# Kernel tuning notes

Measured on AMD Instinct MI355X. Metric: run time of the kernel, lower is better.

## Reference

```python
import jax, jax.numpy as jnp
import numpy as np

H = 31   # hidden_size
IN = 36  # input_size
NC = 7   # num_classes
B = 1024
T = 512


def setup_inputs() -> dict:
    key = jax.random.key(0)
    ks = jax.random.split(key, 19)
    s = 1.0 / np.sqrt(H)  # PyTorch GRU init range
    u = lambda k, shape: jax.random.uniform(k, shape, jnp.float32, -s, s)
    inp = {"x": jax.random.normal(ks[0], (B, T, IN), jnp.float32)}
    i = 1
    for l, din in ((0, IN), (1, 2 * H)):
        for d in ("f", "b"):
            inp[f"W_ih_l{l}{d}"] = u(ks[i], (3 * H, din)); i += 1
            inp[f"W_hh_l{l}{d}"] = u(ks[i], (3 * H, H)); i += 1
            inp[f"b_ih_l{l}{d}"] = u(ks[i], (3 * H,)); i += 1
            inp[f"b_hh_l{l}{d}"] = u(ks[i], (3 * H,)); i += 1
    inp["fc_w"] = u(ks[17], (NC, 2 * H))
    inp["fc_b"] = u(ks[18], (NC,))
    return inp


def _gru_dir(x, Wih, Whh, bih, bhh, reverse):
    # x: [B,T,F]; precompute input-side gates for all timesteps in one GEMM
    xg = jnp.einsum('btf,gf->btg', x, Wih) + bih  # [B,T,3H]
    if reverse:
        xg = xg[:, ::-1]

    def step(h, xt):
        hg = h @ Whh.T + bhh                      # [B,3H]
        xr, xz, xn = jnp.split(xt, 3, axis=-1)    # PyTorch gate order: r,z,n
        hr, hz, hn = jnp.split(hg, 3, axis=-1)
        r = jax.nn.sigmoid(xr + hr)
        z = jax.nn.sigmoid(xz + hz)
        n = jnp.tanh(xn + r * hn)
        h_new = (1.0 - z) * n + z * h
        return h_new, h_new

    h0 = jnp.zeros((x.shape[0], Whh.shape[1]), x.dtype)
    _, ys = jax.lax.scan(step, h0, jnp.swapaxes(xg, 0, 1))  # [T,B,H]
    ys = jnp.swapaxes(ys, 0, 1)                              # [B,T,H]
    return ys[:, ::-1] if reverse else ys


def _forward(x, params, fc_w, fc_b):
    h = x
    for pf, pb in params:  # 2 layers (structural loop)
        yf = _gru_dir(h, *pf, reverse=False)
        yb = _gru_dir(h, *pb, reverse=True)
        h = jnp.concatenate([yf, yb], axis=-1)  # [B,T,2H]
    last = h[:, -1, :]                          # out[:, -1, :]
    return last @ fc_w.T + fc_b                 # [B,NC]


def reference(x, W_ih_l0f, W_hh_l0f, b_ih_l0f, b_hh_l0f,
              W_ih_l0b, W_hh_l0b, b_ih_l0b, b_hh_l0b,
              W_ih_l1f, W_hh_l1f, b_ih_l1f, b_hh_l1f,
              W_ih_l1b, W_hh_l1b, b_ih_l1b, b_hh_l1b,
              fc_w, fc_b):
    params = [((W_ih_l0f, W_hh_l0f, b_ih_l0f, b_hh_l0f),
               (W_ih_l0b, W_hh_l0b, b_ih_l0b, b_hh_l0b)),
              ((W_ih_l1f, W_hh_l1f, b_ih_l1f, b_hh_l1f),
               (W_ih_l1b, W_hh_l1b, b_ih_l1b, b_hh_l1b))]
    return _forward(x, params, fc_w, fc_b)
```

## Files before the change

### kernel.cpp

```cpp
#include <hip/hip_runtime.h>
#include <hip/hip_bf16.h>


#define NB 1024
#define NT 512
#define NH 31
#define NG 93
#define NC 7

__device__ __forceinline__ float sig_(float x) { return 1.f / (1.f + __expf(-x)); }
__device__ __forceinline__ float th_(float x)  { float e = __expf(2.f * x); return (e - 1.f) / (e + 1.f); }

__device__ __forceinline__ float tf_(float v) { return v; }
__device__ __forceinline__ float tf_(__hip_bfloat16 v) { return __bfloat162float(v); }

__device__ __forceinline__ void ldpair(const float* p, float& a, float& b) {
    float2 v = *(const float2*)p; a = v.x; b = v.y;
}
__device__ __forceinline__ void ldpair(const __hip_bfloat16* p, float& a, float& b) {
    ushort2 u = *(const ushort2*)p;
    a = __uint_as_float((unsigned)u.x << 16);
    b = __uint_as_float((unsigned)u.y << 16);
}
__device__ __forceinline__ void stoy(float* p, float v) { *p = v; }
__device__ __forceinline__ void stoy(__hip_bfloat16* p, float v) { *p = __float2bfloat16(v); }

#define PIN(v_) asm volatile("" : "+v"(v_))

#define LOADX(arr, ptr)                                                   \
    _Pragma("unroll") for (int k_ = 0; k_ < KH; k_ += 2)                  \
        ldpair((ptr) + k_, arr[k_], arr[k_ + 1])

#define GRU_STEP(XV)                                                      \
    do {                                                                  \
        const float4 g0 = *(const float4*)&hbuf[w][hlo + 0];              \
        const float4 g1 = *(const float4*)&hbuf[w][hlo + 4];              \
        const float4 g2 = *(const float4*)&hbuf[w][hlo + 8];              \
        const float4 g3 = *(const float4*)&hbuf[w][hlo + 12];             \
        float hv[16];                                                     \
        hv[0]=g0.x;  hv[1]=g0.y;  hv[2]=g0.z;  hv[3]=g0.w;                \
        hv[4]=g1.x;  hv[5]=g1.y;  hv[6]=g1.z;  hv[7]=g1.w;                \
        hv[8]=g2.x;  hv[9]=g2.y;  hv[10]=g2.z; hv[11]=g2.w;               \
        hv[12]=g3.x; hv[13]=g3.y; hv[14]=g3.z; hv[15]=g3.w;               \
        float ar = b_r, az = b_z, an = b_xn, ah = b_hn;                   \
        _Pragma("unroll") for (int k_ = 0; k_ < KH; ++k_) {               \
            ar = fmaf(Wxr[k_], XV[k_], ar);                               \
            az = fmaf(Wxz[k_], XV[k_], az);                               \
            an = fmaf(Wxn[k_], XV[k_], an);                               \
        }                                                                 \
        _Pragma("unroll") for (int k_ = 0; k_ < 16; ++k_) {               \
            ar = fmaf(Whr[k_], hv[k_], ar);                               \
            az = fmaf(Whz[k_], hv[k_], az);                               \
            ah = fmaf(Whn[k_], hv[k_], ah);                               \
        }                                                                 \
        ar += __shfl_xor(ar, 32, 64);                                     \
        az += __shfl_xor(az, 32, 64);                                     \
        an += __shfl_xor(an, 32, 64);                                     \
        ah += __shfl_xor(ah, 32, 64);                                     \
        const float r_ = sig_(ar);                                        \
        const float z_ = sig_(az);                                        \
        const float n_ = th_(an + r_ * ah);                               \
        h_prev = n_ + z_ * (h_prev - n_);                                 \
        if (half == 0 && j < NH) {                                        \
            hbuf[w][j] = h_prev;                                          \
            if (WRITE_Y) stoy(yp, h_prev);                                \
        }                                                                 \
    } while (0)

template<typename XT, typename YT, int DIN, int KH, bool WRITE_Y, bool WRITE_HF>
__device__ __forceinline__ void gru_scan_body(
    const XT* __restrict__ xin,
    const float* __restrict__ Wih, const float* __restrict__ Whh,
    const float* __restrict__ bih, const float* __restrict__ bhh,
    int dir, YT* __restrict__ y, float* __restrict__ hf)
{
    static_assert((KH & 1) == 0, "even KH");
    const int tid  = threadIdx.x;
    const int w    = tid >> 6;
    const int lane = tid & 63;
    const int half = lane >> 5;
    const int j    = lane & 31;
    const int jj   = j < NH ? j : NH - 1;
    const int b    = blockIdx.x * 4 + w;

    __shared__ __align__(16) float hbuf[4][32];
    if (lane < 32) hbuf[w][lane] = 0.f;
    __syncthreads();

    const int klo = half ? (DIN - KH) : 0;

    float Wxr[KH], Wxz[KH], Wxn[KH];
#pragma unroll
    for (int k = 0; k < KH; ++k) {
        const bool v = half ? true : (k < DIN - KH);
        Wxr[k] = v ? Wih[(0 * NH + jj) * DIN + klo + k] : 0.f;
        Wxz[k] = v ? Wih[(1 * NH + jj) * DIN + klo + k] : 0.f;
        Wxn[k] = v ? Wih[(2 * NH + jj) * DIN + klo + k] : 0.f;
        PIN(Wxr[k]); PIN(Wxz[k]); PIN(Wxn[k]);
    }
    const int hlo = half * 16;
    float Whr[16], Whz[16], Whn[16];
#pragma unroll
    for (int k = 0; k < 16; ++k) {
        const bool v = (hlo + k) < NH;
        Whr[k] = v ? Whh[(0 * NH + jj) * NH + hlo + k] : 0.f;
        Whz[k] = v ? Whh[(1 * NH + jj) * NH + hlo + k] : 0.f;
        Whn[k] = v ? Whh[(2 * NH + jj) * NH + hlo + k] : 0.f;
        PIN(Whr[k]); PIN(Whz[k]); PIN(Whn[k]);
    }
    float b_r = 0.f, b_z = 0.f, b_xn = 0.f, b_hn = 0.f;
    if (half == 0) {
        b_r  = bih[jj] + bhh[jj];
        b_z  = bih[NH + jj] + bhh[NH + jj];
        b_xn = bih[2 * NH + jj];
        b_hn = bhh[2 * NH + jj];
    }
    PIN(b_r); PIN(b_z); PIN(b_xn); PIN(b_hn);

    const XT* xrow = xin + (size_t)b * NT * DIN + klo
                   + (dir ? (size_t)(NT - 1) * DIN : 0);
    const ptrdiff_t xstep = dir ? -DIN : DIN;
    YT* yp = nullptr;
    ptrdiff_t ystep = 0;
    if (WRITE_Y) {
        yp = y + (size_t)b * NT * 62 + dir * NH + j
           + (dir ? (size_t)(NT - 1) * 62 : 0);
        ystep = dir ? -62 : 62;
    }

    float h_prev = 0.f;
    float xa[KH], xb[KH];
    LOADX(xa, xrow);
    const XT* xpre = xrow + xstep;

    for (int s = 0; s < NT; s += 2) {
        LOADX(xb, xpre);
        if (s + 2 < NT) xpre += xstep;
        GRU_STEP(xa);
        if (WRITE_Y) yp += ystep;
        LOADX(xa, xpre);
        if (s + 3 < NT) xpre += xstep;
        GRU_STEP(xb);
        if (WRITE_Y) yp += ystep;
    }
    if (WRITE_HF && half == 0 && j < NH) hf[b * NH + j] = h_prev;
}

template<typename YT>
__global__ void __launch_bounds__(256)
__attribute__((amdgpu_waves_per_eu(2, 2)))
gru_scan_l0(
    const float* __restrict__ x,
    const float* __restrict__ Wf, const float* __restrict__ Uf,
    const float* __restrict__ bf, const float* __restrict__ cf,
    const float* __restrict__ Wb, const float* __restrict__ Ub,
    const float* __restrict__ bb, const float* __restrict__ cb,
    YT* __restrict__ y)
{
    const int d = blockIdx.y;
    gru_scan_body<float, YT, 36, 18, true, false>(
        x, d ? Wb : Wf, d ? Ub : Uf, d ? bb : bf, d ? cb : cf, d, y, nullptr);
}

template<typename YT>
__global__ void __launch_bounds__(256)
__attribute__((amdgpu_waves_per_eu(1, 1)))
gru_scan_l1(
    const YT* __restrict__ y0,
    const float* __restrict__ W, const float* __restrict__ U,
    const float* __restrict__ bi, const float* __restrict__ bh,
    float* __restrict__ hf)
{
    gru_scan_body<YT, YT, 62, 32, false, true>(y0, W, U, bi, bh, 0, (YT*)nullptr, hf);
}

template<typename YT>
__global__ void __launch_bounds__(64, 4) gru_final(
    const YT* __restrict__ y0, const float* __restrict__ hf,
    const float* __restrict__ Wih1b, const float* __restrict__ bih1b,
    const float* __restrict__ bhh1b,
    const float* __restrict__ fcw, const float* __restrict__ fcb,
    float* __restrict__ out)
{
    const int b = blockIdx.x;
    const int lane = threadIdx.x;
    __shared__ float row[62];
    __shared__ float xg[NG];
    __shared__ float last[62];
    const YT* yl = y0 + ((size_t)b * NT + (NT - 1)) * 62;
    if (lane < 62) row[lane] = tf_(yl[lane]);
    __syncthreads();
    for (int g = lane; g < NG; g += 64) {
        float a = bih1b[g];
        const float* wr = Wih1b + g * 62;
#pragma unroll
        for (int k = 0; k < 62; ++k) a = fmaf(wr[k], row[k], a);
        xg[g] = a;
    }
    if (lane < NH) last[lane] = hf[b * NH + lane];
    __syncthreads();
    if (lane < NH) {
        const float r = sig_(xg[lane] + bhh1b[lane]);
        const float z = sig_(xg[NH + lane] + bhh1b[NH + lane]);
        const float n = th_(xg[2 * NH + lane] + r * bhh1b[2 * NH + lane]);
        last[NH + lane] = (1.f - z) * n;
    }
    __syncthreads();
    if (lane < NC) {
        float a = fcb[lane];
        const float* wr = fcw + lane * 62;
#pragma unroll
        for (int k = 0; k < 62; ++k) a = fmaf(wr[k], last[k], a);
        out[b * NC + lane] = a;
    }
}

extern "C" void kernel_launch(void* const* d_in, const int* in_sizes, int n_in,
                              void* d_out, int out_size, void* d_ws, size_t ws_size,
                              hipStream_t stream)
{
    const float* x     = (const float*)d_in[0];
    const float* Wih0f = (const float*)d_in[1];
    const float* Whh0f = (const float*)d_in[2];
    const float* bih0f = (const float*)d_in[3];
    const float* bhh0f = (const float*)d_in[4];
    const float* Wih0b = (const float*)d_in[5];
    const float* Whh0b = (const float*)d_in[6];
    const float* bih0b = (const float*)d_in[7];
    const float* bhh0b = (const float*)d_in[8];
    const float* Wih1f = (const float*)d_in[9];
    const float* Whh1f = (const float*)d_in[10];
    const float* bih1f = (const float*)d_in[11];
    const float* bhh1f = (const float*)d_in[12];
    const float* Wih1b = (const float*)d_in[13];
    const float* Whh1b = (const float*)d_in[14];
    const float* bih1b = (const float*)d_in[15];
    const float* bhh1b = (const float*)d_in[16];
    const float* fcw   = (const float*)d_in[17];
    const float* fcb   = (const float*)d_in[18];
    float* out = (float*)d_out;
    (void)Whh1b; (void)in_sizes; (void)n_in; (void)out_size;

    const size_t y0_elems  = (size_t)NB * NT * 62;
    const size_t hf_bytes  = (size_t)NB * NH * 4;
    const size_t need_f32  = y0_elems * 4 + 256 + hf_bytes;
    const size_t need_bf16 = y0_elems * 2 + 256 + hf_bytes;

    const dim3 blk(256);
    if (ws_size >= need_f32) {
        float* y0 = (float*)d_ws;
        float* hf = (float*)((char*)d_ws + ((y0_elems * 4 + 255) & ~(size_t)255));
        gru_scan_l0<float><<<dim3(NB / 4, 2), blk, 0, stream>>>(
            x, Wih0f, Whh0f, bih0f, bhh0f, Wih0b, Whh0b, bih0b, bhh0b, y0);
        gru_scan_l1<float><<<dim3(NB / 4, 1), blk, 0, stream>>>(
            y0, Wih1f, Whh1f, bih1f, bhh1f, hf);
        gru_final<float><<<dim3(NB), dim3(64), 0, stream>>>(
            y0, hf, Wih1b, bih1b, bhh1b, fcw, fcb, out);
    } else if (ws_size >= need_bf16) {
        __hip_bfloat16* y0 = (__hip_bfloat16*)d_ws;
        float* hf = (float*)((char*)d_ws + ((y0_elems * 2 + 255) & ~(size_t)255));
        gru_scan_l0<__hip_bfloat16><<<dim3(NB / 4, 2), blk, 0, stream>>>(
            x, Wih0f, Whh0f, bih0f, bhh0f, Wih0b, Whh0b, bih0b, bhh0b, y0);
        gru_scan_l1<__hip_bfloat16><<<dim3(NB / 4, 1), blk, 0, stream>>>(
            y0, Wih1f, Whh1f, bih1f, bhh1f, hf);
        gru_final<__hip_bfloat16><<<dim3(NB), dim3(64), 0, stream>>>(
            y0, hf, Wih1b, bih1b, bhh1b, fcw, fcb, out);
    }
}
```

Measured before the change: 571.1 us.

## Precompute input-gate projections in separate kernels and run a lean recurrent scan

```diff
diff --git a/kernel.cpp b/kernel.cpp
--- a/kernel.cpp
+++ b/kernel.cpp
@@ -7,6 +7,8 @@
 #define NH 31
 #define NG 93
 #define NC 7
+#define BT (NB * NT)
+#define XGP 96
 
 __device__ __forceinline__ float sig_(float x) { return 1.f / (1.f + __expf(-x)); }
 __device__ __forceinline__ float th_(float x)  { float e = __expf(2.f * x); return (e - 1.f) / (e + 1.f); }
@@ -24,6 +26,232 @@
 }
 __device__ __forceinline__ void stoy(float* p, float v) { *p = v; }
 __device__ __forceinline__ void stoy(__hip_bfloat16* p, float v) { *p = __float2bfloat16(v); }
+
+
+template<int DIN, int NDIR>
+__global__ void __launch_bounds__(256)
+__attribute__((amdgpu_waves_per_eu(1, 4)))
+gru_xg(const float* __restrict__ xin,
+       const float* __restrict__ W0, const float* __restrict__ bi0,
+       const float* __restrict__ W1, const float* __restrict__ bi1,
+       float* __restrict__ xg)
+{
+    __shared__ float tile[256 * DIN];
+    const int tid = threadIdx.x;
+    const size_t blk0 = (size_t)blockIdx.x * 256;
+
+    {
+        const float2* gsrc = (const float2*)(xin + blk0 * DIN);
+        float2* lds2 = (float2*)tile;
+#pragma unroll
+        for (int i = 0; i < DIN / 2; ++i)
+            lds2[tid + i * 256] = gsrc[tid + i * 256];
+    }
+    __syncthreads();
+
+    float xr[DIN];
+#pragma unroll
+    for (int k = 0; k < DIN; k += 2) {
+        float2 v = *(const float2*)&tile[tid * DIN + k];
+        xr[k] = v.x; xr[k + 1] = v.y;
+    }
+    const size_t row = blk0 + tid;
+
+#pragma unroll
+    for (int d = 0; d < NDIR; ++d) {
+        const float* __restrict__ W  = d ? W1 : W0;
+        const float* __restrict__ bi = d ? bi1 : bi0;
+        float* outp = xg + (d * (size_t)BT + row) * XGP;
+        for (int g = 0; g < NG - 1; g += 4) {
+            float a0 = bi[g], a1 = bi[g + 1], a2 = bi[g + 2], a3 = bi[g + 3];
+#pragma unroll
+            for (int k = 0; k < DIN; ++k) {
+                const float xv = xr[k];
+                a0 = fmaf(W[(g + 0) * DIN + k], xv, a0);
+                a1 = fmaf(W[(g + 1) * DIN + k], xv, a1);
+                a2 = fmaf(W[(g + 2) * DIN + k], xv, a2);
+                a3 = fmaf(W[(g + 3) * DIN + k], xv, a3);
+            }
+            float4 o; o.x = a0; o.y = a1; o.z = a2; o.w = a3;
+            *(float4*)(outp + g) = o;
+        }
+        {
+            float a = bi[NG - 1];
+#pragma unroll
+            for (int k = 0; k < DIN; ++k)
+                a = fmaf(W[(NG - 1) * DIN + k], xr[k], a);
+            outp[NG - 1] = a;
+        }
+    }
+}
+
+#define LDG3(R_, Z_, N_, P_)                                              \
+    do { R_ = (P_)[jj]; Z_ = (P_)[NH + jj]; N_ = (P_)[2 * NH + jj]; } while (0)
+
+#define ADVX()                                                            \
+    do { if (++tl < NT) xq += xqs; } while (0)
+
+#define LSTEP(XR_, XZ_, XN_)                                              \
+    do {                                                                  \
+        const float4 q0 = *(const float4*)&hbuf[w][hlo + 0];              \
+        const float4 q1 = *(const float4*)&hbuf[w][hlo + 4];              \
+        const float4 q2 = *(const float4*)&hbuf[w][hlo + 8];              \
+        const float4 q3 = *(const float4*)&hbuf[w][hlo + 12];             \
+        float hv[16];                                                     \
+        hv[0]=q0.x;  hv[1]=q0.y;  hv[2]=q0.z;  hv[3]=q0.w;                \
+        hv[4]=q1.x;  hv[5]=q1.y;  hv[6]=q1.z;  hv[7]=q1.w;                \
+        hv[8]=q2.x;  hv[9]=q2.y;  hv[10]=q2.z; hv[11]=q2.w;               \
+        hv[12]=q3.x; hv[13]=q3.y; hv[14]=q3.z; hv[15]=q3.w;               \
+        float ar = fmaf(hm, XR_, b_r);                                    \
+        float az = fmaf(hm, XZ_, b_z);                                    \
+        float an = hm * (XN_);                                            \
+        float ah = b_hn;                                                  \
+        _Pragma("unroll") for (int k_ = 0; k_ < 16; ++k_) {               \
+            ar = fmaf(Whr[k_], hv[k_], ar);                               \
+            az = fmaf(Whz[k_], hv[k_], az);                               \
+            ah = fmaf(Whn[k_], hv[k_], ah);                               \
+        }                                                                 \
+        ar += __shfl_xor(ar, 32, 64);                                     \
+        az += __shfl_xor(az, 32, 64);                                     \
+        an += __shfl_xor(an, 32, 64);                                     \
+        ah += __shfl_xor(ah, 32, 64);                                     \
+        const float r_ = sig_(ar);                                        \
+        const float z_ = sig_(az);                                        \
+        const float n_ = th_(an + r_ * ah);                               \
+        h_prev = n_ + z_ * (h_prev - n_);                                 \
+        if (half == 0 && j < NH) {                                        \
+            hbuf[w][j] = h_prev;                                          \
+            if (WRITE_Y) *yp = h_prev;                                    \
+        }                                                                 \
+        if (WRITE_Y) yp += ystep;                                         \
+    } while (0)
+
+template<bool WRITE_Y, bool WRITE_HF>
+__device__ __forceinline__ void gru_scan_lean_body(
+    const float* __restrict__ xgd,
+    const float* __restrict__ Whh, const float* __restrict__ bhh,
+    int dir, float* __restrict__ y, float* __restrict__ hf)
+{
+    const int tid  = threadIdx.x;
+    const int w    = tid >> 6;
+    const int lane = tid & 63;
+    const int half = lane >> 5;
+    const int j    = lane & 31;
+    const int jj   = j < NH ? j : NH - 1;
+    const int b    = blockIdx.x * 4 + w;
+
+    __shared__ __align__(16) float hbuf[4][32];
+    if (lane < 32) hbuf[w][lane] = 0.f;
+    __syncthreads();
+
+    const int hlo = half * 16;
+    float Whr[16], Whz[16], Whn[16];
+#pragma unroll
+    for (int k = 0; k < 16; ++k) {
+        const bool v = (hlo + k) < NH;
+        Whr[k] = v ? Whh[(0 * NH + jj) * NH + hlo + k] : 0.f;
+        Whz[k] = v ? Whh[(1 * NH + jj) * NH + hlo + k] : 0.f;
+        Whn[k] = v ? Whh[(2 * NH + jj) * NH + hlo + k] : 0.f;
+    }
+    float b_r = 0.f, b_z = 0.f, b_hn = 0.f;
+    if (half == 0) {
+        b_r  = bhh[jj];
+        b_z  = bhh[NH + jj];
+        b_hn = bhh[2 * NH + jj];
+    }
+    const float hm = (half == 0) ? 1.f : 0.f;
+
+    const float* xq = xgd + ((size_t)b * NT + (dir ? NT - 1 : 0)) * XGP;
+    const ptrdiff_t xqs = dir ? -XGP : XGP;
+    float* yp = nullptr;
+    ptrdiff_t ystep = 0;
+    if (WRITE_Y) {
+        yp = y + (size_t)b * NT * 62 + dir * NH + j
+           + (dir ? (size_t)(NT - 1) * 62 : 0);
+        ystep = dir ? -62 : 62;
+    }
+
+    float h_prev = 0.f;
+    int tl = 0;
+    float ra, za, na, rb, zb, nb, rc, zc, nc, rd, zd, nd;
+    LDG3(ra, za, na, xq); ADVX();
+    LDG3(rb, zb, nb, xq); ADVX();
+    LDG3(rc, zc, nc, xq); ADVX();
+
+    for (int it = 0; it < NT / 4; ++it) {
+        LDG3(rd, zd, nd, xq); ADVX();
+        LSTEP(ra, za, na);
+        LDG3(ra, za, na, xq); ADVX();
+        LSTEP(rb, zb, nb);
+        LDG3(rb, zb, nb, xq); ADVX();
+        LSTEP(rc, zc, nc);
+        LDG3(rc, zc, nc, xq); ADVX();
+        LSTEP(rd, zd, nd);
+    }
+    if (WRITE_HF && half == 0 && j < NH) hf[b * NH + j] = h_prev;
+}
+
+__global__ void __launch_bounds__(256)
+__attribute__((amdgpu_waves_per_eu(2, 2)))
+gru_scan_lean_l0(const float* __restrict__ xg,
+                 const float* __restrict__ Uf, const float* __restrict__ cf,
+                 const float* __restrict__ Ub, const float* __restrict__ cb,
+                 float* __restrict__ y)
+{
+    const int d = blockIdx.y;
+    gru_scan_lean_body<true, false>(xg + (size_t)d * BT * XGP,
+                                    d ? Ub : Uf, d ? cb : cf, d, y, nullptr);
+}
+
+__global__ void __launch_bounds__(256)
+__attribute__((amdgpu_waves_per_eu(1, 1)))
+gru_scan_lean_l1(const float* __restrict__ xg,
+                 const float* __restrict__ U, const float* __restrict__ c,
+                 float* __restrict__ hf)
+{
+    gru_scan_lean_body<false, true>(xg, U, c, 0, nullptr, hf);
+}
+
+__global__ void __launch_bounds__(64, 4) gru_final(
+    const float* __restrict__ y0, const float* __restrict__ hf,
+    const float* __restrict__ Wih1b, const float* __restrict__ bih1b,
+    const float* __restrict__ bhh1b,
+    const float* __restrict__ fcw, const float* __restrict__ fcb,
+    float* __restrict__ out)
+{
+    const int b = blockIdx.x;
+    const int lane = threadIdx.x;
+    __shared__ float row[62];
+    __shared__ float xg[NG];
+    __shared__ float last[62];
+    const float* yl = y0 + ((size_t)b * NT + (NT - 1)) * 62;
+    if (lane < 62) row[lane] = yl[lane];
+    __syncthreads();
+    for (int g = lane; g < NG; g += 64) {
+        float a = bih1b[g];
+        const float* wr = Wih1b + g * 62;
+#pragma unroll
+        for (int k = 0; k < 62; ++k) a = fmaf(wr[k], row[k], a);
+        xg[g] = a;
+    }
+    if (lane < NH) last[lane] = hf[b * NH + lane];
+    __syncthreads();
+    if (lane < NH) {
+        const float r = sig_(xg[lane] + bhh1b[lane]);
+        const float z = sig_(xg[NH + lane] + bhh1b[NH + lane]);
+        const float n = th_(xg[2 * NH + lane] + r * bhh1b[2 * NH + lane]);
+        last[NH + lane] = (1.f - z) * n;
+    }
+    __syncthreads();
+    if (lane < NC) {
+        float a = fcb[lane];
+        const float* wr = fcw + lane * 62;
+#pragma unroll
+        for (int k = 0; k < 62; ++k) a = fmaf(wr[k], last[k], a);
+        out[b * NC + lane] = a;
+    }
+}
+
 
 #define PIN(v_) asm volatile("" : "+v"(v_))
 
@@ -88,7 +316,6 @@
     __syncthreads();
 
     const int klo = half ? (DIN - KH) : 0;
-
     float Wxr[KH], Wxz[KH], Wxn[KH];
 #pragma unroll
     for (int k = 0; k < KH; ++k) {
@@ -149,13 +376,12 @@
 template<typename YT>
 __global__ void __launch_bounds__(256)
 __attribute__((amdgpu_waves_per_eu(2, 2)))
-gru_scan_l0(
-    const float* __restrict__ x,
-    const float* __restrict__ Wf, const float* __restrict__ Uf,
-    const float* __restrict__ bf, const float* __restrict__ cf,
-    const float* __restrict__ Wb, const float* __restrict__ Ub,
-    const float* __restrict__ bb, const float* __restrict__ cb,
-    YT* __restrict__ y)
+gru_scan_l0(const float* __restrict__ x,
+            const float* __restrict__ Wf, const float* __restrict__ Uf,
+            const float* __restrict__ bf, const float* __restrict__ cf,
+            const float* __restrict__ Wb, const float* __restrict__ Ub,
+            const float* __restrict__ bb, const float* __restrict__ cb,
+            YT* __restrict__ y)
 {
     const int d = blockIdx.y;
     gru_scan_body<float, YT, 36, 18, true, false>(
@@ -165,17 +391,16 @@
 template<typename YT>
 __global__ void __launch_bounds__(256)
 __attribute__((amdgpu_waves_per_eu(1, 1)))
-gru_scan_l1(
-    const YT* __restrict__ y0,
-    const float* __restrict__ W, const float* __restrict__ U,
-    const float* __restrict__ bi, const float* __restrict__ bh,
-    float* __restrict__ hf)
+gru_scan_l1(const YT* __restrict__ y0,
+            const float* __restrict__ W, const float* __restrict__ U,
+            const float* __restrict__ bi, const float* __restrict__ bh,
+            float* __restrict__ hf)
 {
     gru_scan_body<YT, YT, 62, 32, false, true>(y0, W, U, bi, bh, 0, (YT*)nullptr, hf);
 }
 
 template<typename YT>
-__global__ void __launch_bounds__(64, 4) gru_final(
+__global__ void __launch_bounds__(64, 4) gru_final_t(
     const YT* __restrict__ y0, const float* __restrict__ hf,
     const float* __restrict__ Wih1b, const float* __restrict__ bih1b,
     const float* __restrict__ bhh1b,
@@ -214,6 +439,7 @@
         out[b * NC + lane] = a;
     }
 }
+
 
 extern "C" void kernel_launch(void* const* d_in, const int* in_sizes, int n_in,
                               void* d_out, int out_size, void* d_ws, size_t ws_size,
@@ -241,20 +467,40 @@
     float* out = (float*)d_out;
     (void)Whh1b; (void)in_sizes; (void)n_in; (void)out_size;
 
-    const size_t y0_elems  = (size_t)NB * NT * 62;
-    const size_t hf_bytes  = (size_t)NB * NH * 4;
+    const size_t y0_bytes = (size_t)BT * 62 * 4;
+    const size_t hf_bytes = (size_t)NB * NH * 4;
+    const size_t xg_bytes = (size_t)2 * BT * XGP * 4;
+    const size_t need_A   = y0_bytes + 256 + hf_bytes + 256 + xg_bytes + 256;
+
+    const size_t y0_elems  = (size_t)BT * 62;
     const size_t need_f32  = y0_elems * 4 + 256 + hf_bytes;
     const size_t need_bf16 = y0_elems * 2 + 256 + hf_bytes;
 
     const dim3 blk(256);
-    if (ws_size >= need_f32) {
+    if (ws_size >= need_A) {
+        char* p = (char*)d_ws;
+        float* y0 = (float*)p;                 p += (y0_bytes + 255) & ~(size_t)255;
+        float* hf = (float*)p;                 p += (hf_bytes + 255) & ~(size_t)255;
+        float* xg = (float*)p;
+
+        gru_xg<36, 2><<<dim3(BT / 256), blk, 0, stream>>>(
+            x, Wih0f, bih0f, Wih0b, bih0b, xg);
+        gru_scan_lean_l0<<<dim3(NB / 4, 2), blk, 0, stream>>>(
+            xg, Whh0f, bhh0f, Whh0b, bhh0b, y0);
+        gru_xg<62, 1><<<dim3(BT / 256), blk, 0, stream>>>(
+            y0, Wih1f, bih1f, nullptr, nullptr, xg);
+        gru_scan_lean_l1<<<dim3(NB / 4), blk, 0, stream>>>(
+            xg, Whh1f, bhh1f, hf);
+        gru_final<<<dim3(NB), dim3(64), 0, stream>>>(
+            y0, hf, Wih1b, bih1b, bhh1b, fcw, fcb, out);
+    } else if (ws_size >= need_f32) {
         float* y0 = (float*)d_ws;
         float* hf = (float*)((char*)d_ws + ((y0_elems * 4 + 255) & ~(size_t)255));
         gru_scan_l0<float><<<dim3(NB / 4, 2), blk, 0, stream>>>(
             x, Wih0f, Whh0f, bih0f, bhh0f, Wih0b, Whh0b, bih0b, bhh0b, y0);
         gru_scan_l1<float><<<dim3(NB / 4, 1), blk, 0, stream>>>(
             y0, Wih1f, Whh1f, bih1f, bhh1f, hf);
-        gru_final<float><<<dim3(NB), dim3(64), 0, stream>>>(
+        gru_final_t<float><<<dim3(NB), dim3(64), 0, stream>>>(
             y0, hf, Wih1b, bih1b, bhh1b, fcw, fcb, out);
     } else if (ws_size >= need_bf16) {
         __hip_bfloat16* y0 = (__hip_bfloat16*)d_ws;
@@ -263,7 +509,7 @@
             x, Wih0f, Whh0f, bih0f, bhh0f, Wih0b, Whh0b, bih0b, bhh0b, y0);
         gru_scan_l1<__hip_bfloat16><<<dim3(NB / 4, 1), blk, 0, stream>>>(
             y0, Wih1f, Whh1f, bih1f, bhh1f, hf);
-        gru_final<__hip_bfloat16><<<dim3(NB), dim3(64), 0, stream>>>(
+        gru_final_t<__hip_bfloat16><<<dim3(NB), dim3(64), 0, stream>>>(
             y0, hf, Wih1b, bih1b, bhh1b, fcw, fcb, out);
     }
 }
```

Measured after the change: 570.4 us. No clear change (-0.1%).
